# Performance work log

Measured on AMD Instinct MI355X. Metric: run time of the kernel, lower is better.

## Reference

```python
import jax, jax.numpy as jnp
import numpy as np

# Layer node counts: [n0, n1, n2, n3] for a 3-hop sampled subgraph
N_NODES = [524288, 65536, 8192, 1024]
DIMS = [100, 256, 256, 47]


def sage_conv(x_src, x_dst, src, dst, Wl, bl, Wr, n_dst):
    # PyG SAGEConv: lin_l(mean_agg(neighbors)) + lin_r(root)
    msg = x_src[src]                                        # [E, in]
    agg = jax.ops.segment_sum(msg, dst, num_segments=n_dst)  # [n_dst, in]
    cnt = jax.ops.segment_sum(jnp.ones((src.shape[0],), dtype=x_src.dtype), dst,
                              num_segments=n_dst)
    agg = agg / jnp.maximum(cnt, 1.0)[:, None]               # mean, 0-deg -> 0
    return agg @ Wl + bl + x_dst @ Wr


def setup_inputs() -> dict:
    key = jax.random.key(0)
    ks = jax.random.split(key, 20)
    inp = {"x": jax.random.normal(ks[0], (N_NODES[0], DIMS[0]), dtype=jnp.float32)}
    E = [655360, 81920, 10240]
    for i in range(3):
        inp[f"src{i}"] = jax.random.randint(ks[1 + 2 * i], (E[i],), 0, N_NODES[i])
        inp[f"dst{i}"] = jax.random.randint(ks[2 + 2 * i], (E[i],), 0, N_NODES[i + 1])
    for i in range(3):
        fin, fout = DIMS[i], DIMS[i + 1]
        inp[f"Wl{i}"] = jax.random.normal(ks[7 + 3 * i], (fin, fout), jnp.float32) * (1.0 / np.sqrt(fin))
        inp[f"bl{i}"] = jnp.zeros((fout,), jnp.float32)
        inp[f"Wr{i}"] = jax.random.normal(ks[8 + 3 * i], (fin, fout), jnp.float32) * (1.0 / np.sqrt(fin))
    return inp


def reference(x, src0, dst0, src1, dst1, src2, dst2,
              Wl0, bl0, Wr0, Wl1, bl1, Wr1, Wl2, bl2, Wr2):
    srcs = [src0, src1, src2]
    dsts = [dst0, dst1, dst2]
    Wls = [Wl0, Wl1, Wl2]
    bls = [bl0, bl1, bl2]
    Wrs = [Wr0, Wr1, Wr2]
    h = x
    for i in range(3):
        n_dst = N_NODES[i + 1]
        h_dst = h[:n_dst]
        h = sage_conv(h, h_dst, srcs[i], dsts[i], Wls[i], bls[i], Wrs[i], n_dst)
        if i != 2:
            h = jax.nn.relu(h)  # dropout is identity in eval mode
    return jax.nn.log_softmax(h, axis=-1)
```

## Files before the change

### kernel.cpp

```cpp
#include <hip/hip_runtime.h>
#include <math.h>

constexpr int NN1 = 65536, NN2 = 8192, NN3 = 1024;
constexpr int E0 = 655360, E1 = 81920, E2 = 10240;
constexpr int ETOT = E0 + E1 + E2;
constexpr int NTOT = NN1 + NN2 + NN3;

static inline int cdiv(int a, int b) { return (a + b - 1) / b; }

typedef __bf16 bf16x8_t __attribute__((ext_vector_type(8)));
typedef float f32x4_t __attribute__((ext_vector_type(4)));

__device__ __forceinline__ unsigned short f2bf(float f) {
    union { float f; unsigned int u; } v; v.f = f;
    unsigned int r = v.u + 0x7fffu + ((v.u >> 16) & 1u);
    return (unsigned short)(r >> 16);
}
__device__ __forceinline__ float bf2f(unsigned short h) {
    union { unsigned int u; float f; } v; v.u = ((unsigned int)h) << 16;
    return v.f;
}

__global__ void count_all(const int* __restrict__ dst0, const int* __restrict__ dst1,
                          const int* __restrict__ dst2, int* __restrict__ cnt) {
    int i = blockIdx.x * 256 + threadIdx.x;
    if (i < E0) atomicAdd(&cnt[dst0[i]], 1);
    else if (i < E0 + E1) atomicAdd(&cnt[NN1 + dst1[i - E0]], 1);
    else if (i < ETOT) atomicAdd(&cnt[NN1 + NN2 + dst2[i - E0 - E1]], 1);
}

__global__ __launch_bounds__(1024) void scan1(const int* __restrict__ cnt, int n,
                                              int* __restrict__ ofs, int* __restrict__ sums) {
    __shared__ int s[1024];
    int i = blockIdx.x * 1024 + threadIdx.x;
    int v = (i < n) ? cnt[i] : 0;
    s[threadIdx.x] = v;
    __syncthreads();
    for (int off = 1; off < 1024; off <<= 1) {
        int t = (threadIdx.x >= off) ? s[threadIdx.x - off] : 0;
        __syncthreads();
        s[threadIdx.x] += t;
        __syncthreads();
    }
    if (i < n) ofs[i] = s[threadIdx.x] - v;
    if (threadIdx.x == 1023) sums[blockIdx.x] = s[1023];
}

__global__ void scan2(int* __restrict__ sums, int nb, int* __restrict__ ofs, int n) {
    __shared__ int s[128];
    int t = threadIdx.x;
    int v = (t < nb) ? sums[t] : 0;
    s[t] = v;
    __syncthreads();
    for (int off = 1; off < 128; off <<= 1) {
        int tv = (t >= off) ? s[t - off] : 0;
        __syncthreads();
        s[t] += tv;
        __syncthreads();
    }
    if (t < nb) sums[t] = s[t] - v;
    if (t == 127) ofs[n] = s[127];
}

__global__ void scan3(const int* __restrict__ sums, int n,
                      int* __restrict__ ofs, int* __restrict__ cursor) {
    int i = blockIdx.x * 256 + threadIdx.x;
    if (i < n) {
        int v = ofs[i] + sums[i >> 10];
        ofs[i] = v;
        cursor[i] = v;
    }
}

__global__ void scatter_all(const int* __restrict__ src0, const int* __restrict__ dst0,
                            const int* __restrict__ src1, const int* __restrict__ dst1,
                            const int* __restrict__ src2, const int* __restrict__ dst2,
                            int* __restrict__ cursor, int* __restrict__ perm) {
    int i = blockIdx.x * 256 + threadIdx.x;
    if (i < E0) {
        int p = atomicAdd(&cursor[dst0[i]], 1);
        perm[p] = src0[i];
    } else if (i < E0 + E1) {
        int j = i - E0;
        int p = atomicAdd(&cursor[NN1 + dst1[j]], 1);
        perm[p] = src1[j];
    } else if (i < ETOT) {
        int j = i - E0 - E1;
        int p = atomicAdd(&cursor[NN1 + NN2 + dst2[j]], 1);
        perm[p] = src2[j];
    }
}

__global__ void agg0_kernel(const float* __restrict__ x, const int* __restrict__ perm,
                            const int* __restrict__ ofs, unsigned short* __restrict__ Ab, int nrows) {
    int wave = (blockIdx.x * blockDim.x + threadIdx.x) >> 6;
    int lane = threadIdx.x & 63;
    if (wave >= nrows) return;
    int s0 = ofs[wave], s1 = ofs[wave + 1];
    float inv = 1.0f / fmaxf((float)(s1 - s0), 1.0f);
    bool act = lane < 25;
    f32x4_t A0 = {0.f, 0.f, 0.f, 0.f}, A1 = A0, A2 = A0, A3 = A0;
    int e = s0;
    for (; e + 4 <= s1; e += 4) {
        int p0 = perm[e], p1 = perm[e + 1], p2 = perm[e + 2], p3 = perm[e + 3];
        if (act) {
            f32x4_t v0 = *reinterpret_cast<const f32x4_t*>(x + (size_t)p0 * 100 + lane * 4);
            f32x4_t v1 = *reinterpret_cast<const f32x4_t*>(x + (size_t)p1 * 100 + lane * 4);
            f32x4_t v2 = *reinterpret_cast<const f32x4_t*>(x + (size_t)p2 * 100 + lane * 4);
            f32x4_t v3 = *reinterpret_cast<const f32x4_t*>(x + (size_t)p3 * 100 + lane * 4);
            A0 += v0; A1 += v1; A2 += v2; A3 += v3;
        }
    }
    for (; e < s1; ++e) {
        int p = perm[e];
        if (act) A0 += *reinterpret_cast<const f32x4_t*>(x + (size_t)p * 100 + lane * 4);
    }
    f32x4_t a = (A0 + A1) + (A2 + A3);
    unsigned short* row = Ab + (size_t)wave * 256;
    ushort4 z = make_ushort4(0, 0, 0, 0);
    if (act) {
        ushort4 o;
        o.x = f2bf(a[0] * inv); o.y = f2bf(a[1] * inv);
        o.z = f2bf(a[2] * inv); o.w = f2bf(a[3] * inv);
        *reinterpret_cast<ushort4*>(row + lane * 4) = o;
        f32x4_t d = *reinterpret_cast<const f32x4_t*>(x + (size_t)wave * 100 + lane * 4);
        ushort4 od;
        od.x = f2bf(d[0]); od.y = f2bf(d[1]); od.z = f2bf(d[2]); od.w = f2bf(d[3]);
        *reinterpret_cast<ushort4*>(row + 128 + lane * 4) = od;
    } else if (lane < 32) {
        *reinterpret_cast<ushort4*>(row + lane * 4) = z;
        *reinterpret_cast<ushort4*>(row + 128 + lane * 4) = z;
    }
}

__global__ void agg1_kernel(const unsigned short* __restrict__ h, const int* __restrict__ perm,
                            const int* __restrict__ ofs, unsigned short* __restrict__ Ab, int nrows) {
    int wave = (blockIdx.x * blockDim.x + threadIdx.x) >> 6;
    int lane = threadIdx.x & 63;
    if (wave >= nrows) return;
    int s0 = ofs[wave], s1 = ofs[wave + 1];
    float inv = 1.0f / fmaxf((float)(s1 - s0), 1.0f);
    float a0 = 0.f, a1 = 0.f, a2 = 0.f, a3 = 0.f;
    float b0 = 0.f, b1 = 0.f, b2 = 0.f, b3 = 0.f;
    int e = s0;
    for (; e + 2 <= s1; e += 2) {
        int p0 = perm[e], p1 = perm[e + 1];
        ushort4 v0 = *reinterpret_cast<const ushort4*>(h + (size_t)p0 * 256 + lane * 4);
        ushort4 v1 = *reinterpret_cast<const ushort4*>(h + (size_t)p1 * 256 + lane * 4);
        a0 += bf2f(v0.x); a1 += bf2f(v0.y); a2 += bf2f(v0.z); a3 += bf2f(v0.w);
        b0 += bf2f(v1.x); b1 += bf2f(v1.y); b2 += bf2f(v1.z); b3 += bf2f(v1.w);
    }
    if (e < s1) {
        ushort4 v = *reinterpret_cast<const ushort4*>(h + (size_t)perm[e] * 256 + lane * 4);
        a0 += bf2f(v.x); a1 += bf2f(v.y); a2 += bf2f(v.z); a3 += bf2f(v.w);
    }
    ushort4 o;
    o.x = f2bf((a0 + b0) * inv); o.y = f2bf((a1 + b1) * inv);
    o.z = f2bf((a2 + b2) * inv); o.w = f2bf((a3 + b3) * inv);
    *reinterpret_cast<ushort4*>(Ab + (size_t)wave * 512 + lane * 4) = o;
    *reinterpret_cast<ushort4*>(Ab + (size_t)wave * 512 + 256 + lane * 4) =
        *reinterpret_cast<const ushort4*>(h + (size_t)wave * 256 + lane * 4);
}

__global__ void agg_vec4_256(const float* __restrict__ x, const int* __restrict__ perm,
                             const int* __restrict__ ofs, float* __restrict__ agg, int nrows) {
    int wave = (blockIdx.x * blockDim.x + threadIdx.x) >> 6;
    int lane = threadIdx.x & 63;
    if (wave >= nrows) return;
    int s0 = ofs[wave], s1 = ofs[wave + 1];
    float4 acc = make_float4(0.f, 0.f, 0.f, 0.f);
    for (int e = s0; e < s1; e++) {
        const float4* xr = (const float4*)(x + (size_t)perm[e] * 256);
        float4 v = xr[lane];
        acc.x += v.x; acc.y += v.y; acc.z += v.z; acc.w += v.w;
    }
    float inv = 1.0f / fmaxf((float)(s1 - s0), 1.0f);
    acc.x *= inv; acc.y *= inv; acc.z *= inv; acc.w *= inv;
    ((float4*)(agg + (size_t)wave * 256))[lane] = acc;
}

__global__ void prep_w0(const float* __restrict__ Wl, const float* __restrict__ Wr,
                        unsigned short* __restrict__ Wt) {
    int idx = blockIdx.x * 256 + threadIdx.x;
    int n = idx >> 8, k = idx & 255;
    float v = 0.f;
    if (k < 100) v = Wl[k * 256 + n];
    else if (k >= 128 && k < 228) v = Wr[(k - 128) * 256 + n];
    Wt[idx] = f2bf(v);
}
__global__ void prep_w1(const float* __restrict__ Wl, const float* __restrict__ Wr,
                        unsigned short* __restrict__ Wt) {
    int idx = blockIdx.x * 256 + threadIdx.x;
    int n = idx >> 9, k = idx & 511;
    float v = (k < 256) ? Wl[k * 256 + n] : Wr[(k - 256) * 256 + n];
    Wt[idx] = f2bf(v);
}

template <int OUT_BF16, int RELU>
__global__ __launch_bounds__(256) void mfma_gemm(const unsigned short* __restrict__ A,
                                                 const unsigned short* __restrict__ Wt,
                                                 const float* __restrict__ bias,
                                                 void* __restrict__ outp,
                                                 int M, int N, int K) {
    __shared__ unsigned short As[128][40];
    __shared__ unsigned short Bs[128][40];
    int tid = threadIdx.x;
    int lane = tid & 63, wid = tid >> 6;
    int wm = (wid & 1) * 64, wn = (wid >> 1) * 64;
    int bm = blockIdx.y * 128, bn = blockIdx.x * 128;

    f32x4_t acc[4][4];
#pragma unroll
    for (int i = 0; i < 4; i++)
#pragma unroll
        for (int j = 0; j < 4; j++)
#pragma unroll
            for (int r = 0; r < 4; r++) acc[i][j][r] = 0.f;

    int r0 = lane & 15, kg = lane >> 4;

    for (int k0 = 0; k0 < K; k0 += 32) {
        {
            int c = tid;
            int row = c >> 2, k8 = (c & 3) << 3;
            *reinterpret_cast<int4*>(&As[row][k8]) =
                *reinterpret_cast<const int4*>(&A[(size_t)(bm + row) * K + k0 + k8]);
            c = tid + 256;
            row = c >> 2; k8 = (c & 3) << 3;
            *reinterpret_cast<int4*>(&As[row][k8]) =
                *reinterpret_cast<const int4*>(&A[(size_t)(bm + row) * K + k0 + k8]);
        }
        {
            int c = tid;
            int row = c >> 2, k8 = (c & 3) << 3;
            *reinterpret_cast<int4*>(&Bs[row][k8]) =
                *reinterpret_cast<const int4*>(&Wt[(size_t)(bn + row) * K + k0 + k8]);
            c = tid + 256;
            row = c >> 2; k8 = (c & 3) << 3;
            *reinterpret_cast<int4*>(&Bs[row][k8]) =
                *reinterpret_cast<const int4*>(&Wt[(size_t)(bn + row) * K + k0 + k8]);
        }
        __syncthreads();

        bf16x8_t af[4], bfv[4];
#pragma unroll
        for (int mi = 0; mi < 4; mi++)
            af[mi] = *reinterpret_cast<const bf16x8_t*>(&As[wm + mi * 16 + r0][kg * 8]);
#pragma unroll
        for (int ni = 0; ni < 4; ni++)
            bfv[ni] = *reinterpret_cast<const bf16x8_t*>(&Bs[wn + ni * 16 + r0][kg * 8]);
#pragma unroll
        for (int mi = 0; mi < 4; mi++)
#pragma unroll
            for (int ni = 0; ni < 4; ni++)
                acc[mi][ni] = __builtin_amdgcn_mfma_f32_16x16x32_bf16(af[mi], bfv[ni], acc[mi][ni], 0, 0, 0);
        __syncthreads();
    }

    int cc = lane & 15, rr = (lane >> 4) * 4;
#pragma unroll
    for (int mi = 0; mi < 4; mi++) {
#pragma unroll
        for (int ni = 0; ni < 4; ni++) {
            int col = bn + wn + ni * 16 + cc;
            float b = bias[col];
#pragma unroll
            for (int j = 0; j < 4; j++) {
                int row = bm + wm + mi * 16 + rr + j;
                float v = acc[mi][ni][j] + b;
                if (RELU) v = fmaxf(v, 0.f);
                if (OUT_BF16)
                    ((unsigned short*)outp)[(size_t)row * N + col] = f2bf(v);
                else
                    ((float*)outp)[(size_t)row * N + col] = v;
            }
        }
    }
}

__global__ __launch_bounds__(256) void gemm2_fused(const float* __restrict__ A1, const float* __restrict__ W1, int K1,
                                                   const float* __restrict__ A2, const float* __restrict__ W2, int K2,
                                                   const float* __restrict__ bias, float* __restrict__ out,
                                                   int M, int N) {
    __shared__ float As[16][65];
    __shared__ float Bs[16][64];
    int tid = threadIdx.x;
    int tx = tid & 15, ty = tid >> 4;
    int bm = blockIdx.y * 64;
    float acc[4][4] = {};
    for (int pass = 0; pass < 2; ++pass) {
        const float* A = pass ? A2 : A1;
        const float* W = pass ? W2 : W1;
        int K = pass ? K2 : K1;
        for (int k0 = 0; k0 < K; k0 += 16) {
#pragma unroll
            for (int i = 0; i < 4; i++) {
                int L = i * 256 + tid;
                int m = L >> 4, k = L & 15;
                int gm = bm + m, gk = k0 + k;
                float v = 0.f;
                if (gm < M && gk < K) v = A[(size_t)gm * K + gk];
                As[k][m] = v;
            }
#pragma unroll
            for (int i = 0; i < 4; i++) {
                int L = i * 256 + tid;
                int n = L & 63, k = L >> 6;
                int gk = k0 + k;
                float v = 0.f;
                if (gk < K && n < N) v = W[(size_t)gk * N + n];
                Bs[k][n] = v;
            }
            __syncthreads();
#pragma unroll
            for (int k = 0; k < 16; k++) {
                float a[4], b[4];
#pragma unroll
                for (int i = 0; i < 4; i++) a[i] = As[k][ty * 4 + i];
#pragma unroll
                for (int j = 0; j < 4; j++) b[j] = Bs[k][tx * 4 + j];
#pragma unroll
                for (int i = 0; i < 4; i++)
#pragma unroll
                    for (int j = 0; j < 4; j++) acc[i][j] += a[i] * b[j];
            }
            __syncthreads();
        }
    }
#pragma unroll
    for (int i = 0; i < 4; i++) {
        int gm = bm + ty * 4 + i;
        float vals[4];
        float vmax = -1e30f;
#pragma unroll
        for (int j = 0; j < 4; j++) {
            int gn = tx * 4 + j;
            vals[j] = (gn < N) ? acc[i][j] + bias[gn] : -1e30f;
            vmax = fmaxf(vmax, vals[j]);
        }
#pragma unroll
        for (int o = 1; o < 16; o <<= 1) vmax = fmaxf(vmax, __shfl_xor(vmax, o));
        float se = 0.f;
#pragma unroll
        for (int j = 0; j < 4; j++) {
            int gn = tx * 4 + j;
            if (gn < N) se += expf(vals[j] - vmax);
        }
#pragma unroll
        for (int o = 1; o < 16; o <<= 1) se += __shfl_xor(se, o);
        float ls = logf(se);
#pragma unroll
        for (int j = 0; j < 4; j++) {
            int gn = tx * 4 + j;
            if (gn < N && gm < M) out[(size_t)gm * N + gn] = vals[j] - vmax - ls;
        }
    }
}

extern "C" void kernel_launch(void* const* d_in, const int* in_sizes, int n_in,
                              void* d_out, int out_size, void* d_ws, size_t ws_size,
                              hipStream_t stream) {
    const float* x   = (const float*)d_in[0];
    const int* src0  = (const int*)d_in[1];
    const int* dst0  = (const int*)d_in[2];
    const int* src1  = (const int*)d_in[3];
    const int* dst1  = (const int*)d_in[4];
    const int* src2  = (const int*)d_in[5];
    const int* dst2  = (const int*)d_in[6];
    const float* Wl0 = (const float*)d_in[7];
    const float* bl0 = (const float*)d_in[8];
    const float* Wr0 = (const float*)d_in[9];
    const float* Wl1 = (const float*)d_in[10];
    const float* bl1 = (const float*)d_in[11];
    const float* Wr1 = (const float*)d_in[12];
    const float* Wl2 = (const float*)d_in[13];
    const float* bl2 = (const float*)d_in[14];
    const float* Wr2 = (const float*)d_in[15];
    float* out = (float*)d_out;

    char* p = (char*)d_ws;
    auto alloc = [&](size_t bytes) { char* r = p; p += (bytes + 255) & ~(size_t)255; return r; };
    unsigned short* Ab0 = (unsigned short*)alloc((size_t)NN1 * 256 * 2);
    unsigned short* h1  = (unsigned short*)alloc((size_t)NN1 * 256 * 2);
    unsigned short* Ab1 = (unsigned short*)alloc((size_t)NN2 * 512 * 2);
    float* h2    = (float*)alloc((size_t)NN2 * 256 * 4);
    float* agg2  = (float*)alloc((size_t)NN3 * 256 * 4);
    unsigned short* Wt0 = (unsigned short*)alloc(256 * 256 * 2);
    unsigned short* Wt1 = (unsigned short*)alloc(256 * 512 * 2);
    int* cnt    = (int*)alloc((size_t)NTOT * 4);
    int* ofs    = (int*)alloc((size_t)(NTOT + 1) * 4);
    int* cursor = (int*)alloc((size_t)(NTOT + 1) * 4);
    int* sums   = (int*)alloc(128 * 4);
    int* perm   = (int*)alloc((size_t)ETOT * 4);

    prep_w0<<<256, 256, 0, stream>>>(Wl0, Wr0, Wt0);
    prep_w1<<<512, 256, 0, stream>>>(Wl1, Wr1, Wt1);
    hipMemsetAsync(cnt, 0, (size_t)NTOT * 4, stream);
    count_all<<<cdiv(ETOT, 256), 256, 0, stream>>>(dst0, dst1, dst2, cnt);
    int nb = cdiv(NTOT, 1024);
    scan1<<<nb, 1024, 0, stream>>>(cnt, NTOT, ofs, sums);
    scan2<<<1, 128, 0, stream>>>(sums, nb, ofs, NTOT);
    scan3<<<cdiv(NTOT, 256), 256, 0, stream>>>(sums, NTOT, ofs, cursor);
    scatter_all<<<cdiv(ETOT, 256), 256, 0, stream>>>(src0, dst0, src1, dst1, src2, dst2, cursor, perm);

    agg0_kernel<<<cdiv(NN1 * 64, 256), 256, 0, stream>>>(x, perm, ofs, Ab0, NN1);
    {
        dim3 grid(256 / 128, NN1 / 128);
        mfma_gemm<1, 1><<<grid, 256, 0, stream>>>(Ab0, Wt0, bl0, h1, NN1, 256, 256);
    }

    agg1_kernel<<<cdiv(NN2 * 64, 256), 256, 0, stream>>>(h1, perm, ofs + NN1, Ab1, NN2);
    {
        dim3 grid(256 / 128, NN2 / 128);
        mfma_gemm<0, 1><<<grid, 256, 0, stream>>>(Ab1, Wt1, bl1, h2, NN2, 256, 512);
    }

    agg_vec4_256<<<cdiv(NN3 * 64, 256), 256, 0, stream>>>(h2, perm, ofs + NN1 + NN2, agg2, NN3);
    {
        dim3 grid(1, cdiv(NN3, 64));
        gemm2_fused<<<grid, 256, 0, stream>>>(agg2, Wl2, 256, h2, Wr2, 256, bl2, out, NN3, 47);
    }
}
```

Before: 309.0 us.

## Pack layer-0 K to 224, split waves in agg0, merge prep and scan launches

```diff
diff --git a/kernel.cpp b/kernel.cpp
--- a/kernel.cpp
+++ b/kernel.cpp
@@ -46,30 +46,24 @@
     if (threadIdx.x == 1023) sums[blockIdx.x] = s[1023];
 }
 
-__global__ void scan2(int* __restrict__ sums, int nb, int* __restrict__ ofs, int n) {
-    __shared__ int s[128];
-    int t = threadIdx.x;
-    int v = (t < nb) ? sums[t] : 0;
-    s[t] = v;
-    __syncthreads();
-    for (int off = 1; off < 128; off <<= 1) {
-        int tv = (t >= off) ? s[t - off] : 0;
-        __syncthreads();
-        s[t] += tv;
-        __syncthreads();
-    }
-    if (t < nb) sums[t] = s[t] - v;
-    if (t == 127) ofs[n] = s[127];
-}
-
 __global__ void scan3(const int* __restrict__ sums, int n,
                       int* __restrict__ ofs, int* __restrict__ cursor) {
+    __shared__ int pref_s;
+    int c = (blockIdx.x * 256) >> 10;
+    if (threadIdx.x < 64) {
+        int v = 0;
+        for (int j = threadIdx.x; j < c; j += 64) v += sums[j];
+        for (int o = 32; o; o >>= 1) v += __shfl_down(v, o);
+        if (threadIdx.x == 0) pref_s = v;
+    }
+    __syncthreads();
     int i = blockIdx.x * 256 + threadIdx.x;
     if (i < n) {
-        int v = ofs[i] + sums[i >> 10];
+        int v = ofs[i] + pref_s;
         ofs[i] = v;
         cursor[i] = v;
     }
+    if (blockIdx.x == 0 && threadIdx.x == 0) ofs[n] = ETOT;
 }
 
 __global__ void scatter_all(const int* __restrict__ src0, const int* __restrict__ dst0,
@@ -96,29 +90,34 @@
     int wave = (blockIdx.x * blockDim.x + threadIdx.x) >> 6;
     int lane = threadIdx.x & 63;
     if (wave >= nrows) return;
+    int g = lane >> 5, l5 = lane & 31;
+    bool act = l5 < 25;
     int s0 = ofs[wave], s1 = ofs[wave + 1];
     float inv = 1.0f / fmaxf((float)(s1 - s0), 1.0f);
-    bool act = lane < 25;
     f32x4_t A0 = {0.f, 0.f, 0.f, 0.f}, A1 = A0, A2 = A0, A3 = A0;
     int e = s0;
-    for (; e + 4 <= s1; e += 4) {
-        int p0 = perm[e], p1 = perm[e + 1], p2 = perm[e + 2], p3 = perm[e + 3];
+    for (; e + 8 <= s1; e += 8) {
+        int p0 = perm[e + 0 + g];
+        int p1 = perm[e + 2 + g];
+        int p2 = perm[e + 4 + g];
+        int p3 = perm[e + 6 + g];
         if (act) {
-            f32x4_t v0 = *reinterpret_cast<const f32x4_t*>(x + (size_t)p0 * 100 + lane * 4);
-            f32x4_t v1 = *reinterpret_cast<const f32x4_t*>(x + (size_t)p1 * 100 + lane * 4);
-            f32x4_t v2 = *reinterpret_cast<const f32x4_t*>(x + (size_t)p2 * 100 + lane * 4);
-            f32x4_t v3 = *reinterpret_cast<const f32x4_t*>(x + (size_t)p3 * 100 + lane * 4);
-            A0 += v0; A1 += v1; A2 += v2; A3 += v3;
-        }
-    }
-    for (; e < s1; ++e) {
-        int p = perm[e];
-        if (act) A0 += *reinterpret_cast<const f32x4_t*>(x + (size_t)p * 100 + lane * 4);
+            A0 += *reinterpret_cast<const f32x4_t*>(x + (size_t)p0 * 100 + l5 * 4);
+            A1 += *reinterpret_cast<const f32x4_t*>(x + (size_t)p1 * 100 + l5 * 4);
+            A2 += *reinterpret_cast<const f32x4_t*>(x + (size_t)p2 * 100 + l5 * 4);
+            A3 += *reinterpret_cast<const f32x4_t*>(x + (size_t)p3 * 100 + l5 * 4);
+        }
+    }
+    for (; e < s1; e += 2) {
+        int idx = e + g;
+        if (idx < s1 && act)
+            A0 += *reinterpret_cast<const f32x4_t*>(x + (size_t)perm[idx] * 100 + l5 * 4);
     }
     f32x4_t a = (A0 + A1) + (A2 + A3);
-    unsigned short* row = Ab + (size_t)wave * 256;
-    ushort4 z = make_ushort4(0, 0, 0, 0);
-    if (act) {
+#pragma unroll
+    for (int c = 0; c < 4; c++) a[c] += __shfl_xor(a[c], 32);
+    unsigned short* row = Ab + (size_t)wave * 224;
+    if (lane < 25) {
         ushort4 o;
         o.x = f2bf(a[0] * inv); o.y = f2bf(a[1] * inv);
         o.z = f2bf(a[2] * inv); o.w = f2bf(a[3] * inv);
@@ -126,10 +125,9 @@
         f32x4_t d = *reinterpret_cast<const f32x4_t*>(x + (size_t)wave * 100 + lane * 4);
         ushort4 od;
         od.x = f2bf(d[0]); od.y = f2bf(d[1]); od.z = f2bf(d[2]); od.w = f2bf(d[3]);
-        *reinterpret_cast<ushort4*>(row + 128 + lane * 4) = od;
-    } else if (lane < 32) {
-        *reinterpret_cast<ushort4*>(row + lane * 4) = z;
-        *reinterpret_cast<ushort4*>(row + 128 + lane * 4) = z;
+        *reinterpret_cast<ushort4*>(row + 100 + lane * 4) = od;
+    } else if (lane < 31) {
+        *reinterpret_cast<ushort4*>(row + 100 + lane * 4) = make_ushort4(0, 0, 0, 0);
     }
 }
 
@@ -140,23 +138,29 @@
     if (wave >= nrows) return;
     int s0 = ofs[wave], s1 = ofs[wave + 1];
     float inv = 1.0f / fmaxf((float)(s1 - s0), 1.0f);
-    float a0 = 0.f, a1 = 0.f, a2 = 0.f, a3 = 0.f;
-    float b0 = 0.f, b1 = 0.f, b2 = 0.f, b3 = 0.f;
+    float acc[4][4] = {};
     int e = s0;
-    for (; e + 2 <= s1; e += 2) {
-        int p0 = perm[e], p1 = perm[e + 1];
-        ushort4 v0 = *reinterpret_cast<const ushort4*>(h + (size_t)p0 * 256 + lane * 4);
-        ushort4 v1 = *reinterpret_cast<const ushort4*>(h + (size_t)p1 * 256 + lane * 4);
-        a0 += bf2f(v0.x); a1 += bf2f(v0.y); a2 += bf2f(v0.z); a3 += bf2f(v0.w);
-        b0 += bf2f(v1.x); b1 += bf2f(v1.y); b2 += bf2f(v1.z); b3 += bf2f(v1.w);
-    }
-    if (e < s1) {
+    for (; e + 4 <= s1; e += 4) {
+        ushort4 v[4];
+#pragma unroll
+        for (int u = 0; u < 4; u++)
+            v[u] = *reinterpret_cast<const ushort4*>(h + (size_t)perm[e + u] * 256 + lane * 4);
+#pragma unroll
+        for (int u = 0; u < 4; u++) {
+            acc[u][0] += bf2f(v[u].x); acc[u][1] += bf2f(v[u].y);
+            acc[u][2] += bf2f(v[u].z); acc[u][3] += bf2f(v[u].w);
+        }
+    }
+    for (; e < s1; e++) {
         ushort4 v = *reinterpret_cast<const ushort4*>(h + (size_t)perm[e] * 256 + lane * 4);
-        a0 += bf2f(v.x); a1 += bf2f(v.y); a2 += bf2f(v.z); a3 += bf2f(v.w);
+        acc[0][0] += bf2f(v.x); acc[0][1] += bf2f(v.y);
+        acc[0][2] += bf2f(v.z); acc[0][3] += bf2f(v.w);
     }
     ushort4 o;
-    o.x = f2bf((a0 + b0) * inv); o.y = f2bf((a1 + b1) * inv);
-    o.z = f2bf((a2 + b2) * inv); o.w = f2bf((a3 + b3) * inv);
+    o.x = f2bf((acc[0][0] + acc[1][0] + acc[2][0] + acc[3][0]) * inv);
+    o.y = f2bf((acc[0][1] + acc[1][1] + acc[2][1] + acc[3][1]) * inv);
+    o.z = f2bf((acc[0][2] + acc[1][2] + acc[2][2] + acc[3][2]) * inv);
+    o.w = f2bf((acc[0][3] + acc[1][3] + acc[2][3] + acc[3][3]) * inv);
     *reinterpret_cast<ushort4*>(Ab + (size_t)wave * 512 + lane * 4) = o;
     *reinterpret_cast<ushort4*>(Ab + (size_t)wave * 512 + 256 + lane * 4) =
         *reinterpret_cast<const ushort4*>(h + (size_t)wave * 256 + lane * 4);
@@ -179,21 +183,23 @@
     ((float4*)(agg + (size_t)wave * 256))[lane] = acc;
 }
 
-__global__ void prep_w0(const float* __restrict__ Wl, const float* __restrict__ Wr,
-                        unsigned short* __restrict__ Wt) {
-    int idx = blockIdx.x * 256 + threadIdx.x;
-    int n = idx >> 8, k = idx & 255;
-    float v = 0.f;
-    if (k < 100) v = Wl[k * 256 + n];
-    else if (k >= 128 && k < 228) v = Wr[(k - 128) * 256 + n];
-    Wt[idx] = f2bf(v);
-}
-__global__ void prep_w1(const float* __restrict__ Wl, const float* __restrict__ Wr,
-                        unsigned short* __restrict__ Wt) {
-    int idx = blockIdx.x * 256 + threadIdx.x;
-    int n = idx >> 9, k = idx & 511;
-    float v = (k < 256) ? Wl[k * 256 + n] : Wr[(k - 256) * 256 + n];
-    Wt[idx] = f2bf(v);
+__global__ void prep_w(const float* __restrict__ Wl0, const float* __restrict__ Wr0,
+                       unsigned short* __restrict__ Wt0,
+                       const float* __restrict__ Wl1, const float* __restrict__ Wr1,
+                       unsigned short* __restrict__ Wt1) {
+    int b = blockIdx.x;
+    if (b < 256) {
+        int n = b, k = threadIdx.x;
+        if (k < 224) {
+            float v = (k < 100) ? Wl0[k * 256 + n] : (k < 200 ? Wr0[(k - 100) * 256 + n] : 0.f);
+            Wt0[n * 224 + k] = f2bf(v);
+        }
+    } else {
+        int idx = (b - 256) * 256 + threadIdx.x;
+        int n = idx >> 9, k = idx & 511;
+        float v = (k < 256) ? Wl1[k * 256 + n] : Wr1[(k - 256) * 256 + n];
+        Wt1[idx] = f2bf(v);
+    }
 }
 
 template <int OUT_BF16, int RELU>
@@ -380,12 +386,12 @@
 
     char* p = (char*)d_ws;
     auto alloc = [&](size_t bytes) { char* r = p; p += (bytes + 255) & ~(size_t)255; return r; };
-    unsigned short* Ab0 = (unsigned short*)alloc((size_t)NN1 * 256 * 2);
+    unsigned short* Ab0 = (unsigned short*)alloc((size_t)NN1 * 224 * 2);
     unsigned short* h1  = (unsigned short*)alloc((size_t)NN1 * 256 * 2);
     unsigned short* Ab1 = (unsigned short*)alloc((size_t)NN2 * 512 * 2);
     float* h2    = (float*)alloc((size_t)NN2 * 256 * 4);
     float* agg2  = (float*)alloc((size_t)NN3 * 256 * 4);
-    unsigned short* Wt0 = (unsigned short*)alloc(256 * 256 * 2);
+    unsigned short* Wt0 = (unsigned short*)alloc(256 * 224 * 2);
     unsigned short* Wt1 = (unsigned short*)alloc(256 * 512 * 2);
     int* cnt    = (int*)alloc((size_t)NTOT * 4);
     int* ofs    = (int*)alloc((size_t)(NTOT + 1) * 4);
@@ -393,20 +399,18 @@
     int* sums   = (int*)alloc(128 * 4);
     int* perm   = (int*)alloc((size_t)ETOT * 4);
 
-    prep_w0<<<256, 256, 0, stream>>>(Wl0, Wr0, Wt0);
-    prep_w1<<<512, 256, 0, stream>>>(Wl1, Wr1, Wt1);
+    prep_w<<<768, 256, 0, stream>>>(Wl0, Wr0, Wt0, Wl1, Wr1, Wt1);
     hipMemsetAsync(cnt, 0, (size_t)NTOT * 4, stream);
     count_all<<<cdiv(ETOT, 256), 256, 0, stream>>>(dst0, dst1, dst2, cnt);
     int nb = cdiv(NTOT, 1024);
     scan1<<<nb, 1024, 0, stream>>>(cnt, NTOT, ofs, sums);
-    scan2<<<1, 128, 0, stream>>>(sums, nb, ofs, NTOT);
     scan3<<<cdiv(NTOT, 256), 256, 0, stream>>>(sums, NTOT, ofs, cursor);
     scatter_all<<<cdiv(ETOT, 256), 256, 0, stream>>>(src0, dst0, src1, dst1, src2, dst2, cursor, perm);
 
     agg0_kernel<<<cdiv(NN1 * 64, 256), 256, 0, stream>>>(x, perm, ofs, Ab0, NN1);
     {
         dim3 grid(256 / 128, NN1 / 128);
-        mfma_gemm<1, 1><<<grid, 256, 0, stream>>>(Ab0, Wt0, bl0, h1, NN1, 256, 256);
+        mfma_gemm<1, 1><<<grid, 256, 0, stream>>>(Ab0, Wt0, bl0, h1, NN1, 256, 224);
     }
 
     agg1_kernel<<<cdiv(NN2 * 64, 256), 256, 0, stream>>>(h1, perm, ofs + NN1, Ab1, NN2);
```

Result: faster. 298.8 us (-3.3%).
